# Optimization experiments

Hardware: AMD Instinct MI355X
Metric: run time of the kernel (lower is better)

The kernel has to match this reference:

```python
import jax, jax.numpy as jnp
import numpy as np

N, E, D, C, H1 = 50000, 800000, 128, 8, 2


def setup_inputs() -> dict:
    key = jax.random.key(0)
    ks = jax.random.split(key, 14)
    s = lambda k, sh: (jax.random.normal(k, sh, jnp.float32) * 0.05)
    return {
        "x": jax.random.normal(ks[0], (N, D), jnp.float32),
        "edge_index": jax.random.randint(ks[1], (2, E), 0, N, dtype=jnp.int32),
        # conv1: GATConv(D, D, heads=2, concat=True)
        "W1": s(ks[2], (D, H1 * D)),
        "att1_src": s(ks[3], (H1, D)),
        "att1_dst": s(ks[4], (H1, D)),
        "b1": s(ks[5], (H1 * D,)),
        # conv2: GATConv(2D, D, heads=1, concat=False)
        "W2": s(ks[6], (H1 * D, D)),
        "att2_src": s(ks[7], (1, D)),
        "att2_dst": s(ks[8], (1, D)),
        "b2": s(ks[9], (D,)),
        # MLP head
        "Wm1": s(ks[10], (D, D)),
        "bm1": s(ks[11], (D,)),
        "Wm2": s(ks[12], (D, C)),
        "bm2": s(ks[13], (C,)),
    }


def gat_conv(x, src, dst, W, a_src, a_dst, b, heads, out_ch, concat):
    """PyG GATConv (eval mode): self-loops added by caller, softmax over
    edges grouped by destination node, negative_slope=0.2."""
    n = x.shape[0]
    h = (x @ W).reshape(n, heads, out_ch)              # [N,H,F]
    alpha_src = jnp.einsum('nhf,hf->nh', h, a_src)     # [N,H]
    alpha_dst = jnp.einsum('nhf,hf->nh', h, a_dst)     # [N,H]
    e = jax.nn.leaky_relu(alpha_src[src] + alpha_dst[dst], 0.2)  # [E,H]
    e_max = jax.ops.segment_max(e, dst, num_segments=n)
    ex = jnp.exp(e - e_max[dst])
    denom = jax.ops.segment_sum(ex, dst, num_segments=n)
    alpha = ex / jnp.maximum(denom[dst], 1e-16)        # [E,H]
    out = jax.ops.segment_sum(h[src] * alpha[:, :, None], dst, num_segments=n)
    out = out.reshape(n, heads * out_ch) if concat else out.mean(axis=1)
    return out + b


def reference(x, edge_index, W1, att1_src, att1_dst, b1,
              W2, att2_src, att2_dst, b2, Wm1, bm1, Wm2, bm2):
    n = x.shape[0]
    loop = jnp.arange(n, dtype=edge_index.dtype)
    src = jnp.concatenate([edge_index[0], loop])  # add_self_loops=True
    dst = jnp.concatenate([edge_index[1], loop])
    h = jax.nn.elu(gat_conv(x, src, dst, W1, att1_src, att1_dst, b1, H1, D, True))
    h = jax.nn.elu(gat_conv(h, src, dst, W2, att2_src, att2_dst, b2, 1, D, False))
    h = jax.nn.relu(h @ Wm1 + bm1)
    return jax.nn.relu(h @ Wm2 + bm2)
```

## Files before the change

### kernel.cpp

```cpp
#include <hip/hip_runtime.h>
#include <hip/hip_bf16.h>


__device__ __forceinline__ float lrelu(float x){ return x > 0.f ? x : 0.2f*x; }
__device__ __forceinline__ float elu_f(float x){ return x > 0.f ? x : __expf(x) - 1.f; }
__device__ __forceinline__ unsigned short f2bf(float f){
  __hip_bfloat16 h = __float2bfloat16(f);
  return *reinterpret_cast<unsigned short*>(&h);
}
__device__ __forceinline__ float bflo(unsigned int u){ return __uint_as_float(u << 16); }
__device__ __forceinline__ float bfhi(unsigned int u){ return __uint_as_float(u & 0xffff0000u); }
__device__ __forceinline__ unsigned int packbf(float a, float b){
  return (unsigned int)f2bf(a) | ((unsigned int)f2bf(b) << 16);
}

typedef __attribute__((ext_vector_type(8))) short bf16x8;
typedef __attribute__((ext_vector_type(4))) float f32x4;

__global__ void prep_kernel(const float* __restrict__ W1, unsigned short* __restrict__ BT1a,
                            unsigned short* __restrict__ BT1b,
                            const float* __restrict__ W2, unsigned short* __restrict__ BT2,
                            const float* __restrict__ Wm1, unsigned short* __restrict__ BT3,
                            const float* __restrict__ a1s, const float* __restrict__ a1d,
                            float* __restrict__ va, int* __restrict__ bcount,
                            int* __restrict__ gcur, int NB){
  int idx = blockIdx.x*256 + threadIdx.x;
  const int S1 = 128*256, S2 = 128*256, S3 = 128*128;
  if (idx < S1){
    int k = idx >> 8, c = idx & 255;
    unsigned short v = f2bf(W1[idx]);
    if (c < 128) BT1a[c*128 + k] = v;
    else         BT1b[(c-128)*128 + k] = v;
  } else if (idx < S1 + S2){
    int j = idx - S1;
    int k = j >> 7, n = j & 127;
    BT2[n*256 + k] = f2bf(W2[j]);
  } else if (idx < S1 + S2 + S3){
    int j = idx - S1 - S2;
    int k = j >> 7, n = j & 127;
    BT3[n*128 + k] = f2bf(Wm1[j]);
  } else if (idx < S1 + S2 + S3 + 512){
    int j = idx - S1 - S2 - S3;
    int v = j >> 7, k = j & 127;
    const float* avec = (v < 2) ? a1s : a1d;
    int head = v & 1;
    const float4* wrow = (const float4*)(W1 + (size_t)k*256 + head*128);
    const float4* arow = (const float4*)(avec + head*128);
    float s = 0.f;
    #pragma unroll 8
    for (int f = 0; f < 32; ++f){
      float4 w = wrow[f], a = arow[f];
      s += w.x*a.x + w.y*a.y + w.z*a.z + w.w*a.w;
    }
    va[j] = s;
  } else if (idx < S1 + S2 + S3 + 512 + 2048){
    int z = idx - (S1 + S2 + S3 + 512);
    if (z < 1024){ if (z < NB) bcount[z] = 0; }
    else { z -= 1024; if (z < NB) gcur[z] = 0; }
  }
}

__global__ __launch_bounds__(256) void f2bf_hist_kernel(
    const float* __restrict__ x, unsigned short* __restrict__ xb, int N,
    const float* __restrict__ va, float* __restrict__ as1, float* __restrict__ ad1,
    const int* __restrict__ dst, int E, int* __restrict__ bcount, int NB, int nbConv)
{
  __shared__ int h[1024];
  if ((int)blockIdx.x < nbConv){
    int i = blockIdx.x*256 + threadIdx.x;
    int total = N*32;
    float4 v = make_float4(0.f,0.f,0.f,0.f);
    if (i < total){
      v = ((const float4*)x)[i];
      ushort4 u; u.x=f2bf(v.x); u.y=f2bf(v.y); u.z=f2bf(v.z); u.w=f2bf(v.w);
      ((ushort4*)xb)[i] = u;
    }
    int c = (i & 31) << 2;
    float4 vs0 = *(const float4*)(va + c);
    float4 vs1 = *(const float4*)(va + 128 + c);
    float4 vd0 = *(const float4*)(va + 256 + c);
    float4 vd1 = *(const float4*)(va + 384 + c);
    float s0 = v.x*vs0.x + v.y*vs0.y + v.z*vs0.z + v.w*vs0.w;
    float s1 = v.x*vs1.x + v.y*vs1.y + v.z*vs1.z + v.w*vs1.w;
    float d0 = v.x*vd0.x + v.y*vd0.y + v.z*vd0.z + v.w*vd0.w;
    float d1 = v.x*vd1.x + v.y*vd1.y + v.z*vd1.z + v.w*vd1.w;
    #pragma unroll
    for (int m = 1; m <= 16; m <<= 1){
      s0 += __shfl_xor(s0, m); s1 += __shfl_xor(s1, m);
      d0 += __shfl_xor(d0, m); d1 += __shfl_xor(d1, m);
    }
    if ((i & 31) == 0 && i < total){
      int n = i >> 5;
      *(float2*)(as1 + 2*n) = make_float2(s0, s1);
      *(float2*)(ad1 + 2*n) = make_float2(d0, d1);
    }
  } else {
    for (int i = threadIdx.x; i < NB; i += 256) h[i] = 0;
    __syncthreads();
    int b0 = blockIdx.x - nbConv;
    for (int e = b0*256 + threadIdx.x; e < E; e += 64*256)
      atomicAdd(&h[dst[e] >> 6], 1);
    __syncthreads();
    for (int i = threadIdx.x; i < NB; i += 256)
      if (h[i]) atomicAdd(&bcount[i], h[i]);
  }
}

__global__ __launch_bounds__(256) void bscatter_kernel(
    const int* __restrict__ src, const int* __restrict__ dst, int E,
    const int* __restrict__ bcount, int* __restrict__ boff,
    int* __restrict__ gcur, unsigned int* __restrict__ pairs, int NB)
{
  __shared__ int h[1024];
  __shared__ int runbase[1024];
  __shared__ int sc[1024];
  const int t = threadIdx.x;
  const int e0 = blockIdx.x * 4096;

  for (int i = t; i < 1024; i += 256) sc[i] = (i < NB) ? bcount[i] : 0;
  for (int i = t; i < NB; i += 256) h[i] = 0;
  __syncthreads();
  for (int d = 1; d < 1024; d <<= 1){
    int v0 = (t       >= d) ? sc[t       - d] : 0;
    int v1 = (t + 256 >= d) ? sc[t + 256 - d] : 0;
    int v2 = (t + 512 >= d) ? sc[t + 512 - d] : 0;
    int v3 = (t + 768 >= d) ? sc[t + 768 - d] : 0;
    __syncthreads();
    sc[t] += v0; sc[t+256] += v1; sc[t+512] += v2; sc[t+768] += v3;
    __syncthreads();
  }
  if (blockIdx.x == 0){
    for (int i = t; i <= NB; i += 256) boff[i] = i ? sc[i-1] : 0;
  }

  int myb[16]; unsigned int myw[16];
  #pragma unroll
  for (int q = 0; q < 16; ++q){
    int e = e0 + q*256 + t;
    int b = -1; unsigned int w = 0;
    if (e < E){
      int d = dst[e];
      b = d >> 6;
      w = ((unsigned int)(d & 63) << 26) | (unsigned int)src[e];
      atomicAdd(&h[b], 1);
    }
    myb[q] = b; myw[q] = w;
  }
  __syncthreads();
  for (int i = t; i < NB; i += 256)
    runbase[i] = h[i] ? atomicAdd(&gcur[i], h[i]) : 0;
  __syncthreads();
  for (int i = t; i < NB; i += 256) h[i] = 0;
  __syncthreads();
  #pragma unroll
  for (int q = 0; q < 16; ++q){
    if (myb[q] >= 0){
      int off = atomicAdd(&h[myb[q]], 1);
      int base = myb[q] ? sc[myb[q]-1] : 0;
      pairs[(size_t)base + runbase[myb[q]] + off] = myw[q];
    }
  }
}

__global__ __launch_bounds__(256) void bbuild_kernel(
    const unsigned int* __restrict__ pairs, const int* __restrict__ boff,
    int* __restrict__ rowptr, int* __restrict__ csr, int N)
{
  __shared__ int deg[64], offs[64], cur[64];
  const int b = blockIdx.x;
  const int t = threadIdx.x;
  const int n0 = b << 6;
  const int nNodes = min(64, N - n0);
  const int p0 = boff[b], p1 = boff[b+1];
  const int base = p0 + n0;
  if (t < 64) deg[t] = (t < nNodes) ? 1 : 0;
  __syncthreads();
  for (int i = p0 + t; i < p1; i += 256)
    atomicAdd(&deg[pairs[i] >> 26], 1);
  __syncthreads();
  if (t < 64){
    int x = deg[t];
    #pragma unroll
    for (int d = 1; d < 64; d <<= 1){
      int y = __shfl_up(x, d);
      if (t >= d) x += y;
    }
    offs[t] = x - deg[t];
    cur[t] = 1;
    if (t < nNodes){
      rowptr[n0 + t + 1] = base + x;
      csr[base + x - deg[t]] = n0 + t;
    }
    if (b == 0 && t == 0) rowptr[0] = 0;
  }
  __syncthreads();
  for (int i = p0 + t; i < p1; i += 256){
    unsigned int w = pairs[i];
    int dl = w >> 26;
    int s  = (int)(w & 0x03ffffffu);
    int off = atomicAdd(&cur[dl], 1);
    csr[base + offs[dl] + off] = s;
  }
}

__device__ __forceinline__ void gemm_core(
    const unsigned short* __restrict__ A, int lda,
    const unsigned short* __restrict__ BT, int M, int K, int r0,
    unsigned short* a_s, unsigned short* b_s, f32x4 (&acc)[4][4])
{
  const int tid  = threadIdx.x;
  const int lane = tid & 63, wv = tid >> 6;
  const int mh = (wv & 1)*64, nh = (wv >> 1)*64;
  const int l15 = lane & 15, quad = lane >> 4;
  const int srow = tid >> 3, skc = tid & 7;

  #pragma unroll
  for (int i = 0; i < 4; ++i)
    #pragma unroll
    for (int j = 0; j < 4; ++j)
      #pragma unroll
      for (int r = 0; r < 4; ++r) acc[i][j][r] = 0.f;

  for (int k0 = 0; k0 < K; k0 += 64){
    #pragma unroll
    for (int it = 0; it < 4; ++it){
      int row = it*32 + srow;
      int grow = r0 + row;
      uint4 v = make_uint4(0u,0u,0u,0u);
      if (grow < M) v = *(const uint4*)(A + (size_t)grow*lda + k0 + skc*8);
      *(uint4*)(&a_s[row*72 + skc*8]) = v;
    }
    #pragma unroll
    for (int it = 0; it < 4; ++it){
      int row = it*32 + srow;
      uint4 v = *(const uint4*)(BT + (size_t)row*K + k0 + skc*8);
      *(uint4*)(&b_s[row*72 + skc*8]) = v;
    }
    __syncthreads();
    #pragma unroll
    for (int ks = 0; ks < 64; ks += 32){
      bf16x8 af[4], bfr[4];
      #pragma unroll
      for (int i = 0; i < 4; ++i)
        af[i] = *(const bf16x8*)(&a_s[(mh + i*16 + l15)*72 + ks + quad*8]);
      #pragma unroll
      for (int j = 0; j < 4; ++j)
        bfr[j] = *(const bf16x8*)(&b_s[(nh + j*16 + l15)*72 + ks + quad*8]);
      #pragma unroll
      for (int i = 0; i < 4; ++i)
        #pragma unroll
        for (int j = 0; j < 4; ++j)
          acc[i][j] = __builtin_amdgcn_mfma_f32_16x16x32_bf16(bfr[j], af[i], acc[i][j], 0, 0, 0);
    }
    __syncthreads();
  }
}

__global__ __launch_bounds__(512, 2) void gemm_conv12_kernel(
    const unsigned short* __restrict__ xa,
    const unsigned short* __restrict__ BT1a, const unsigned short* __restrict__ BT1b,
    const float* __restrict__ b1, const unsigned short* __restrict__ BT2,
    unsigned short* __restrict__ h2b, int M,
    const float* __restrict__ a2s, const float* __restrict__ a2d,
    float* __restrict__ as2, float* __restrict__ ad2)
{
  __shared__ unsigned short t_s[64*264];
  __shared__ unsigned short a_s[64*72];
  __shared__ unsigned short b_s[128*72];
  __shared__ float part_s[64][4];
  __shared__ float part_d[64][4];

  const int tid = threadIdx.x;
  const int lane = tid & 63, wv = tid >> 6;
  const int l15 = lane & 15, quad = lane >> 4;
  const int r0 = blockIdx.x*64;
  const int mh = (wv & 1)*32;
  const int nhp = (wv >> 1)*32;

  const int arow = tid >> 3, askc = tid & 7;
  const int brow = tid >> 2, bc2 = (tid & 3)*2;
  #pragma unroll
  for (int h = 0; h < 2; ++h){
    const unsigned short* BT = h ? BT1b : BT1a;
    f32x4 acc[2][2];
    #pragma unroll
    for (int i = 0; i < 2; ++i)
      #pragma unroll
      for (int j = 0; j < 2; ++j)
        #pragma unroll
        for (int r = 0; r < 4; ++r) acc[i][j][r] = 0.f;

    for (int k0 = 0; k0 < 128; k0 += 64){
      {
        int grow = r0 + arow;
        uint4 v = make_uint4(0u,0u,0u,0u);
        if (grow < M) v = *(const uint4*)(xa + (size_t)grow*256 + h*128 + k0 + askc*8);
        *(uint4*)(&a_s[arow*72 + askc*8]) = v;
      }
      {
        *(uint4*)(&b_s[brow*72 + bc2*8])     = *(const uint4*)(BT + (size_t)brow*128 + k0 + bc2*8);
        *(uint4*)(&b_s[brow*72 + (bc2+1)*8]) = *(const uint4*)(BT + (size_t)brow*128 + k0 + (bc2+1)*8);
      }
      __syncthreads();
      #pragma unroll
      for (int ks = 0; ks < 64; ks += 32){
        bf16x8 af[2], bfr[2];
        #pragma unroll
        for (int i = 0; i < 2; ++i)
          af[i] = *(const bf16x8*)(&a_s[(mh + i*16 + l15)*72 + ks + quad*8]);
        #pragma unroll
        for (int j = 0; j < 2; ++j)
          bfr[j] = *(const bf16x8*)(&b_s[(nhp + j*16 + l15)*72 + ks + quad*8]);
        #pragma unroll
        for (int i = 0; i < 2; ++i)
          #pragma unroll
          for (int j = 0; j < 2; ++j)
            acc[i][j] = __builtin_amdgcn_mfma_f32_16x16x32_bf16(bfr[j], af[i], acc[i][j], 0, 0, 0);
      }
      __syncthreads();
    }
    #pragma unroll
    for (int i = 0; i < 2; ++i){
      int row = mh + i*16 + l15;
      #pragma unroll
      for (int j = 0; j < 2; ++j){
        int n = nhp + j*16 + quad*4;
        float4 bb = *(const float4*)(b1 + h*128 + n);
        ushort4 u;
        u.x = f2bf(elu_f(acc[i][j][0] + bb.x));
        u.y = f2bf(elu_f(acc[i][j][1] + bb.y));
        u.z = f2bf(elu_f(acc[i][j][2] + bb.z));
        u.w = f2bf(elu_f(acc[i][j][3] + bb.w));
        *(ushort4*)(&t_s[row*264 + h*128 + n]) = u;
      }
    }
  }
  __syncthreads();

  f32x4 acc2[2][2];
  #pragma unroll
  for (int i = 0; i < 2; ++i)
    #pragma unroll
    for (int j = 0; j < 2; ++j)
      #pragma unroll
      for (int r = 0; r < 4; ++r) acc2[i][j][r] = 0.f;

  for (int k0 = 0; k0 < 256; k0 += 64){
    {
      *(uint4*)(&b_s[brow*72 + bc2*8])     = *(const uint4*)(BT2 + (size_t)brow*256 + k0 + bc2*8);
      *(uint4*)(&b_s[brow*72 + (bc2+1)*8]) = *(const uint4*)(BT2 + (size_t)brow*256 + k0 + (bc2+1)*8);
    }
    __syncthreads();
    #pragma unroll
    for (int ks = 0; ks < 64; ks += 32){
      bf16x8 af[2], bfr[2];
      #pragma unroll
      for (int i = 0; i < 2; ++i)
        af[i] = *(const bf16x8*)(&t_s[(mh + i*16 + l15)*264 + k0 + ks + quad*8]);
      #pragma unroll
      for (int j = 0; j < 2; ++j)
        bfr[j] = *(const bf16x8*)(&b_s[(nhp + j*16 + l15)*72 + ks + quad*8]);
      #pragma unroll
      for (int i = 0; i < 2; ++i)
        #pragma unroll
        for (int j = 0; j < 2; ++j)
          acc2[i][j] = __builtin_amdgcn_mfma_f32_16x16x32_bf16(bfr[j], af[i], acc2[i][j], 0, 0, 0);
    }
    __syncthreads();
  }

  #pragma unroll
  for (int i = 0; i < 2; ++i){
    int m = r0 + mh + i*16 + l15;
    float ps = 0.f, pd = 0.f;
    #pragma unroll
    for (int j = 0; j < 2; ++j){
      int n = nhp + j*16 + quad*4;
      float4 wsv = *(const float4*)(a2s + n);
      float4 wdv = *(const float4*)(a2d + n);
      float v0 = acc2[i][j][0], v1 = acc2[i][j][1], v2 = acc2[i][j][2], v3 = acc2[i][j][3];
      ps += v0*wsv.x + v1*wsv.y + v2*wsv.z + v3*wsv.w;
      pd += v0*wdv.x + v1*wdv.y + v2*wdv.z + v3*wdv.w;
      if (m < M){
        ushort4 u;
        u.x = f2bf(v0); u.y = f2bf(v1); u.z = f2bf(v2); u.w = f2bf(v3);
        *(ushort4*)(h2b + (size_t)m*128 + n) = u;
      }
    }
    ps += __shfl_xor(ps, 16); ps += __shfl_xor(ps, 32);
    pd += __shfl_xor(pd, 16); pd += __shfl_xor(pd, 32);
    if (quad == 0){
      part_s[mh + i*16 + l15][wv >> 1] = ps;
      part_d[mh + i*16 + l15][wv >> 1] = pd;
    }
  }
  __syncthreads();
  if (tid < 64){
    int gm = r0 + tid;
    if (gm < M){
      as2[gm] = part_s[tid][0] + part_s[tid][1] + part_s[tid][2] + part_s[tid][3];
      ad2[gm] = part_d[tid][0] + part_d[tid][1] + part_d[tid][2] + part_d[tid][3];
    }
  }
}

__global__ __launch_bounds__(256) void gemm_mlp_kernel(
    const unsigned short* __restrict__ gb, const unsigned short* __restrict__ BT3,
    int M, const float* __restrict__ bm1, const float* __restrict__ Wm2,
    const float* __restrict__ bm2, float* __restrict__ out)
{
  __shared__ unsigned short a_s[128*72];
  __shared__ unsigned short b_s[128*72];
  __shared__ float wm2_s[128*8];
  __shared__ float part[128][2][8];
  const int tid = threadIdx.x;
  {
    int i4 = tid*4;
    *(float4*)(&wm2_s[i4]) = *(const float4*)(Wm2 + i4);
  }
  const int r0 = blockIdx.y*128;
  f32x4 acc[4][4];
  gemm_core(gb, 128, BT3, M, 128, r0, a_s, b_s, acc);

  const int lane = tid & 63, wv = tid >> 6;
  const int mh = (wv & 1)*64, nh = (wv >> 1)*64;
  const int l15 = lane & 15, quad = lane >> 4;
  #pragma unroll
  for (int i = 0; i < 4; ++i){
    float po[8];
    #pragma unroll
    for (int o = 0; o < 8; ++o) po[o] = 0.f;
    #pragma unroll
    for (int j = 0; j < 4; ++j){
      int n = nh + j*16 + quad*4;
      float4 bb = *(const float4*)(bm1 + n);
      #pragma unroll
      for (int r = 0; r < 4; ++r){
        float hcol = fmaxf(acc[i][j][r] + ((const float*)&bb)[r], 0.f);
        const float* wr = &wm2_s[(n + r)*8];
        #pragma unroll
        for (int o = 0; o < 8; ++o) po[o] += hcol*wr[o];
      }
    }
    #pragma unroll
    for (int o = 0; o < 8; ++o){
      po[o] += __shfl_xor(po[o], 16);
      po[o] += __shfl_xor(po[o], 32);
    }
    if (quad == 0){
      #pragma unroll
      for (int o = 0; o < 8; ++o) part[mh + i*16 + l15][wv >> 1][o] = po[o];
    }
  }
  __syncthreads();
  if (tid < 128){
    int gm = r0 + tid;
    if (gm < M){
      float4 o0, o1;
      o0.x = fmaxf(part[tid][0][0] + part[tid][1][0] + bm2[0], 0.f);
      o0.y = fmaxf(part[tid][0][1] + part[tid][1][1] + bm2[1], 0.f);
      o0.z = fmaxf(part[tid][0][2] + part[tid][1][2] + bm2[2], 0.f);
      o0.w = fmaxf(part[tid][0][3] + part[tid][1][3] + bm2[3], 0.f);
      o1.x = fmaxf(part[tid][0][4] + part[tid][1][4] + bm2[4], 0.f);
      o1.y = fmaxf(part[tid][0][5] + part[tid][1][5] + bm2[5], 0.f);
      o1.z = fmaxf(part[tid][0][6] + part[tid][1][6] + bm2[6], 0.f);
      o1.w = fmaxf(part[tid][0][7] + part[tid][1][7] + bm2[7], 0.f);
      *(float4*)(out + (size_t)gm*8)     = o0;
      *(float4*)(out + (size_t)gm*8 + 4) = o1;
    }
  }
}

#define AGG1_FMA(u, a0v, a1v) do{ \
    float f0 = bflo(u.x), f1 = bfhi(u.x), f2v = bflo(u.y), f3 = bfhi(u.y); \
    float f4 = bflo(u.z), f5 = bfhi(u.z), f6 = bflo(u.w), f7 = bfhi(u.w); \
    acc0[0] += a0v*f0; acc0[1] += a0v*f1; acc0[2] += a0v*f2v; acc0[3] += a0v*f3; \
    acc0[4] += a0v*f4; acc0[5] += a0v*f5; acc0[6] += a0v*f6;  acc0[7] += a0v*f7; \
    acc1[0] += a1v*f0; acc1[1] += a1v*f1; acc1[2] += a1v*f2v; acc1[3] += a1v*f3; \
    acc1[4] += a1v*f4; acc1[5] += a1v*f5; acc1[6] += a1v*f6;  acc1[7] += a1v*f7; \
  }while(0)

#define AGG2_FMA(u, av) do{ \
    acc[0] += av*bflo(u.x); acc[1] += av*bfhi(u.x); \
    acc[2] += av*bflo(u.y); acc[3] += av*bfhi(u.y); \
    acc[4] += av*bflo(u.z); acc[5] += av*bfhi(u.z); \
    acc[6] += av*bflo(u.w); acc[7] += av*bfhi(u.w); \
  }while(0)

__global__ __launch_bounds__(256) void agg1x_kernel(
    const unsigned short* __restrict__ xb, const float* __restrict__ as_,
    const float* __restrict__ ad_, const int* __restrict__ rowptr, const int* __restrict__ csr,
    unsigned short* __restrict__ xa, int N)
{
  const int wv = threadIdx.x >> 6, lane = threadIdx.x & 63;
  const int ql = lane & 15;
  const int n = blockIdx.x*16 + wv*4 + (lane >> 4);
  const bool valid = n < N;
  int start = 0, end = 0;
  float2 adv = make_float2(0.f, 0.f);
  if (valid){ start = rowptr[n]; end = rowptr[n+1]; adv = *(const float2*)(ad_ + 2*n); }

  int jl = start + ql;
  bool have = valid && (jl < end);
  int s_l = 0;
  float p0 = 0.f, p1 = 0.f;
  if (have){
    s_l = csr[jl];
    float2 av = *(const float2*)(as_ + 2*s_l);
    p0 = __expf(lrelu(av.x + adv.x));
    p1 = __expf(lrelu(av.y + adv.y));
  }
  float l0 = p0, l1 = p1;
  for (int j = jl + 16; j < end; j += 16){
    int s = csr[j];
    float2 av = *(const float2*)(as_ + 2*s);
    l0 += __expf(lrelu(av.x + adv.x));
    l1 += __expf(lrelu(av.y + adv.y));
  }
  #pragma unroll
  for (int msk = 1; msk <= 8; msk <<= 1){
    l0 += __shfl_xor(l0, msk);
    l1 += __shfl_xor(l1, msk);
  }
  float inv0 = 1.f / fmaxf(l0, 1e-16f);
  float inv1 = 1.f / fmaxf(l1, 1e-16f);
  float a0_l = p0 * inv0;
  float a1_l = p1 * inv1;

  float acc0[8], acc1[8];
  #pragma unroll
  for (int i = 0; i < 8; ++i){ acc0[i] = 0.f; acc1[i] = 0.f; }
  const int c = ql << 3;
  const unsigned short* hp = xb + c;

  #pragma unroll
  for (int half = 0; half < 2; ++half){
    uint4 u[8]; float b0[8], b1[8];
    #pragma unroll
    for (int t = 0; t < 8; ++t){
      int tt = half*8 + t;
      int sA = __shfl(s_l, tt, 16);
      b0[t] = __shfl(a0_l, tt, 16);
      b1[t] = __shfl(a1_l, tt, 16);
      u[t] = *(const uint4*)(hp + (sA << 7));
    }
    #pragma unroll
    for (int t = 0; t < 8; ++t) AGG1_FMA(u[t], b0[t], b1[t]);
  }
  for (int jb = start + 16; jb < end; jb += 16){
    int jl2 = jb + ql;
    int s2 = 0; float a0_2 = 0.f, a1_2 = 0.f;
    if (jl2 < end){
      s2 = csr[jl2];
      float2 av = *(const float2*)(as_ + 2*s2);
      a0_2 = __expf(lrelu(av.x + adv.x)) * inv0;
      a1_2 = __expf(lrelu(av.y + adv.y)) * inv1;
    }
    int cnt2 = min(16, end - jb);
    for (int t2 = 0; t2 < cnt2; t2 += 2){
      int   sA  = __shfl(s2, t2, 16),   sB  = __shfl(s2, t2+1, 16);
      float a0A = __shfl(a0_2, t2, 16), a0B = __shfl(a0_2, t2+1, 16);
      float a1A = __shfl(a1_2, t2, 16), a1B = __shfl(a1_2, t2+1, 16);
      uint4 uA = *(const uint4*)(hp + (sA << 7));
      uint4 uB = *(const uint4*)(hp + (sB << 7));
      AGG1_FMA(uA, a0A, a1A);
      AGG1_FMA(uB, a0B, a1B);
    }
  }

  if (valid){
    uint4 u0, u1;
    u0.x = packbf(acc0[0], acc0[1]); u0.y = packbf(acc0[2], acc0[3]);
    u0.z = packbf(acc0[4], acc0[5]); u0.w = packbf(acc0[6], acc0[7]);
    u1.x = packbf(acc1[0], acc1[1]); u1.y = packbf(acc1[2], acc1[3]);
    u1.z = packbf(acc1[4], acc1[5]); u1.w = packbf(acc1[6], acc1[7]);
    *(uint4*)(xa + (size_t)n*256 + c)       = u0;
    *(uint4*)(xa + (size_t)n*256 + 128 + c) = u1;
  }
}

__global__ __launch_bounds__(256) void agg2_kernel(
    const unsigned short* __restrict__ h2b, const float* __restrict__ as_,
    const float* __restrict__ ad_, const int* __restrict__ rowptr, const int* __restrict__ csr,
    const float* __restrict__ b2, unsigned short* __restrict__ outb, int N)
{
  const int wv = threadIdx.x >> 6, lane = threadIdx.x & 63;
  const int ql = lane & 15;
  const int n = blockIdx.x*16 + wv*4 + (lane >> 4);
  const bool valid = n < N;
  int start = 0, end = 0;
  float adn = 0.f;
  if (valid){ start = rowptr[n]; end = rowptr[n+1]; adn = ad_[n]; }

  int jl = start + ql;
  bool have = valid && (jl < end);
  int s_l = 0;
  float p_l = 0.f;
  if (have){
    s_l = csr[jl];
    p_l = __expf(lrelu(as_[s_l] + adn));
  }
  float l = p_l;
  for (int j = jl + 16; j < end; j += 16)
    l += __expf(lrelu(as_[csr[j]] + adn));
  #pragma unroll
  for (int msk = 1; msk <= 8; msk <<= 1) l += __shfl_xor(l, msk);
  float inv = 1.f / fmaxf(l, 1e-16f);
  float a_l = p_l * inv;

  float acc[8];
  #pragma unroll
  for (int i = 0; i < 8; ++i) acc[i] = 0.f;
  const int c = ql << 3;
  const unsigned short* hp = h2b + c;

  #pragma unroll
  for (int half = 0; half < 2; ++half){
    uint4 u[8]; float av[8];
    #pragma unroll
    for (int t = 0; t < 8; ++t){
      int tt = half*8 + t;
      int sA = __shfl(s_l, tt, 16);
      av[t] = __shfl(a_l, tt, 16);
      u[t] = *(const uint4*)(hp + (sA << 7));
    }
    #pragma unroll
    for (int t = 0; t < 8; ++t) AGG2_FMA(u[t], av[t]);
  }
  for (int jb = start + 16; jb < end; jb += 16){
    int jl2 = jb + ql;
    int s2 = 0; float a2 = 0.f;
    if (jl2 < end){
      s2 = csr[jl2];
      a2 = __expf(lrelu(as_[s2] + adn)) * inv;
    }
    int cnt2 = min(16, end - jb);
    for (int t2 = 0; t2 < cnt2; t2 += 2){
      int   sA = __shfl(s2, t2, 16),  sB = __shfl(s2, t2+1, 16);
      float aA = __shfl(a2, t2, 16),  aB = __shfl(a2, t2+1, 16);
      uint4 uA = *(const uint4*)(hp + (sA << 7));
      uint4 uB = *(const uint4*)(hp + (sB << 7));
      AGG2_FMA(uA, aA);
      AGG2_FMA(uB, aB);
    }
  }

  if (valid){
    float4 bb0 = *(const float4*)(b2 + c);
    float4 bb1 = *(const float4*)(b2 + c + 4);
    float o[8];
    o[0]=elu_f(acc[0]+bb0.x); o[1]=elu_f(acc[1]+bb0.y);
    o[2]=elu_f(acc[2]+bb0.z); o[3]=elu_f(acc[3]+bb0.w);
    o[4]=elu_f(acc[4]+bb1.x); o[5]=elu_f(acc[5]+bb1.y);
    o[6]=elu_f(acc[6]+bb1.z); o[7]=elu_f(acc[7]+bb1.w);
    uint4 up;
    up.x = packbf(o[0], o[1]); up.y = packbf(o[2], o[3]);
    up.z = packbf(o[4], o[5]); up.w = packbf(o[6], o[7]);
    *(uint4*)(outb + (size_t)n*128 + c) = up;
  }
}

extern "C" void kernel_launch(void* const* d_in, const int* in_sizes, int n_in,
                              void* d_out, int out_size, void* d_ws, size_t ws_size,
                              hipStream_t stream)
{
  (void)n_in; (void)out_size; (void)ws_size;
  const float* x   = (const float*)d_in[0];
  const int*   ei  = (const int*)d_in[1];
  const float* W1  = (const float*)d_in[2];
  const float* a1s = (const float*)d_in[3];
  const float* a1d = (const float*)d_in[4];
  const float* b1  = (const float*)d_in[5];
  const float* W2  = (const float*)d_in[6];
  const float* a2s = (const float*)d_in[7];
  const float* a2d = (const float*)d_in[8];
  const float* b2  = (const float*)d_in[9];
  const float* Wm1 = (const float*)d_in[10];
  const float* bm1 = (const float*)d_in[11];
  const float* Wm2 = (const float*)d_in[12];
  const float* bm2 = (const float*)d_in[13];
  float* out = (float*)d_out;

  const int N = in_sizes[0] / 128;
  const int E = in_sizes[1] / 2;
  const int NB = (N + 63) >> 6;
  const int* srcp = ei;
  const int* dstp = ei + E;

  char* ws = (char*)d_ws;
  unsigned short* xb    = (unsigned short*)ws;
  unsigned short* xa    = (unsigned short*)(ws + (size_t)N*256);
  unsigned short* h2b   = (unsigned short*)(ws + (size_t)N*768);
  char* tail = ws + (size_t)N*1024;
  unsigned short* BT1a = (unsigned short*)tail;
  unsigned short* BT1b = BT1a + 128*128;
  unsigned short* BT2  = BT1b + 128*128;
  unsigned short* BT3  = BT2 + 128*256;
  float* va   = (float*)(BT3 + 128*128);
  float* as1  = va + 512;
  float* ad1  = as1 + (size_t)2*N;
  float* as2  = ad1 + (size_t)2*N;
  float* ad2  = as2 + N;
  int* bcount = (int*)(ad2 + N);
  int* boff   = bcount + 1024;
  int* gcur   = boff + 1032;
  int* rowptr = gcur + 1024;
  int* csr    = rowptr + N + 1;
  unsigned int* pairs = (unsigned int*)(csr + E + N);

  unsigned short* gb = xb;

  const int nbConv = (N*32 + 255)/256;
  const int prepTotal = 128*256 + 128*256 + 128*128 + 512 + 2048;

  prep_kernel<<<(prepTotal + 255)/256, 256, 0, stream>>>(
      W1, BT1a, BT1b, W2, BT2, Wm1, BT3, a1s, a1d, va, bcount, gcur, NB);
  f2bf_hist_kernel<<<nbConv + 64, 256, 0, stream>>>(x, xb, N, va, as1, ad1,
                                                    dstp, E, bcount, NB, nbConv);
  bscatter_kernel<<<(E + 4095)/4096, 256, 0, stream>>>(srcp, dstp, E, bcount, boff, gcur, pairs, NB);
  bbuild_kernel<<<NB, 256, 0, stream>>>(pairs, boff, rowptr, csr, N);

  const int nb16 = (N + 15) / 16;
  const int g64  = (N + 63) / 64;
  const int gy   = (N + 127) / 128;

  agg1x_kernel<<<nb16, 256, 0, stream>>>(xb, as1, ad1, rowptr, csr, xa, N);
  gemm_conv12_kernel<<<g64, 512, 0, stream>>>(xa, BT1a, BT1b, b1, BT2,
                                              h2b, N, a2s, a2d, as2, ad2);
  agg2_kernel<<<nb16, 256, 0, stream>>>(h2b, as2, ad2, rowptr, csr, b2, gb, N);
  gemm_mlp_kernel<<<dim3(1, gy), 256, 0, stream>>>(gb, BT3, N, bm1, Wm2, bm2, out);
}
```

Measured before the change: 250.9 us.

## Fuse second-layer aggregation with MLP head into a single kernel

Merges the conv2 aggregation kernel and the MLP GEMM kernel. Each 16-node block now writes its ELU'd bf16 features to shared memory and immediately runs a small MFMA GEMM against Wm1, followed by the Wm2 projection. This removes the global write and re-read of the intermediate feature matrix and one kernel launch. In exchange, every block re-reads Wm1 (BT3) from global/L2, the 16-row MFMA tiles are less efficient, and extra shared memory per block may lower occupancy.

```diff
diff --git a/kernel.cpp b/kernel.cpp
--- a/kernel.cpp
+++ b/kernel.cpp
@@ -203,59 +203,6 @@
   }
 }
 
-__device__ __forceinline__ void gemm_core(
-    const unsigned short* __restrict__ A, int lda,
-    const unsigned short* __restrict__ BT, int M, int K, int r0,
-    unsigned short* a_s, unsigned short* b_s, f32x4 (&acc)[4][4])
-{
-  const int tid  = threadIdx.x;
-  const int lane = tid & 63, wv = tid >> 6;
-  const int mh = (wv & 1)*64, nh = (wv >> 1)*64;
-  const int l15 = lane & 15, quad = lane >> 4;
-  const int srow = tid >> 3, skc = tid & 7;
-
-  #pragma unroll
-  for (int i = 0; i < 4; ++i)
-    #pragma unroll
-    for (int j = 0; j < 4; ++j)
-      #pragma unroll
-      for (int r = 0; r < 4; ++r) acc[i][j][r] = 0.f;
-
-  for (int k0 = 0; k0 < K; k0 += 64){
-    #pragma unroll
-    for (int it = 0; it < 4; ++it){
-      int row = it*32 + srow;
-      int grow = r0 + row;
-      uint4 v = make_uint4(0u,0u,0u,0u);
-      if (grow < M) v = *(const uint4*)(A + (size_t)grow*lda + k0 + skc*8);
-      *(uint4*)(&a_s[row*72 + skc*8]) = v;
-    }
-    #pragma unroll
-    for (int it = 0; it < 4; ++it){
-      int row = it*32 + srow;
-      uint4 v = *(const uint4*)(BT + (size_t)row*K + k0 + skc*8);
-      *(uint4*)(&b_s[row*72 + skc*8]) = v;
-    }
-    __syncthreads();
-    #pragma unroll
-    for (int ks = 0; ks < 64; ks += 32){
-      bf16x8 af[4], bfr[4];
-      #pragma unroll
-      for (int i = 0; i < 4; ++i)
-        af[i] = *(const bf16x8*)(&a_s[(mh + i*16 + l15)*72 + ks + quad*8]);
-      #pragma unroll
-      for (int j = 0; j < 4; ++j)
-        bfr[j] = *(const bf16x8*)(&b_s[(nh + j*16 + l15)*72 + ks + quad*8]);
-      #pragma unroll
-      for (int i = 0; i < 4; ++i)
-        #pragma unroll
-        for (int j = 0; j < 4; ++j)
-          acc[i][j] = __builtin_amdgcn_mfma_f32_16x16x32_bf16(bfr[j], af[i], acc[i][j], 0, 0, 0);
-    }
-    __syncthreads();
-  }
-}
-
 __global__ __launch_bounds__(512, 2) void gemm_conv12_kernel(
     const unsigned short* __restrict__ xa,
     const unsigned short* __restrict__ BT1a, const unsigned short* __restrict__ BT1b,
@@ -404,73 +351,6 @@
   }
 }
 
-__global__ __launch_bounds__(256) void gemm_mlp_kernel(
-    const unsigned short* __restrict__ gb, const unsigned short* __restrict__ BT3,
-    int M, const float* __restrict__ bm1, const float* __restrict__ Wm2,
-    const float* __restrict__ bm2, float* __restrict__ out)
-{
-  __shared__ unsigned short a_s[128*72];
-  __shared__ unsigned short b_s[128*72];
-  __shared__ float wm2_s[128*8];
-  __shared__ float part[128][2][8];
-  const int tid = threadIdx.x;
-  {
-    int i4 = tid*4;
-    *(float4*)(&wm2_s[i4]) = *(const float4*)(Wm2 + i4);
-  }
-  const int r0 = blockIdx.y*128;
-  f32x4 acc[4][4];
-  gemm_core(gb, 128, BT3, M, 128, r0, a_s, b_s, acc);
-
-  const int lane = tid & 63, wv = tid >> 6;
-  const int mh = (wv & 1)*64, nh = (wv >> 1)*64;
-  const int l15 = lane & 15, quad = lane >> 4;
-  #pragma unroll
-  for (int i = 0; i < 4; ++i){
-    float po[8];
-    #pragma unroll
-    for (int o = 0; o < 8; ++o) po[o] = 0.f;
-    #pragma unroll
-    for (int j = 0; j < 4; ++j){
-      int n = nh + j*16 + quad*4;
-      float4 bb = *(const float4*)(bm1 + n);
-      #pragma unroll
-      for (int r = 0; r < 4; ++r){
-        float hcol = fmaxf(acc[i][j][r] + ((const float*)&bb)[r], 0.f);
-        const float* wr = &wm2_s[(n + r)*8];
-        #pragma unroll
-        for (int o = 0; o < 8; ++o) po[o] += hcol*wr[o];
-      }
-    }
-    #pragma unroll
-    for (int o = 0; o < 8; ++o){
-      po[o] += __shfl_xor(po[o], 16);
-      po[o] += __shfl_xor(po[o], 32);
-    }
-    if (quad == 0){
-      #pragma unroll
-      for (int o = 0; o < 8; ++o) part[mh + i*16 + l15][wv >> 1][o] = po[o];
-    }
-  }
-  __syncthreads();
-  if (tid < 128){
-    int gm = r0 + tid;
-    if (gm < M){
-      float4 o0, o1;
-      o0.x = fmaxf(part[tid][0][0] + part[tid][1][0] + bm2[0], 0.f);
-      o0.y = fmaxf(part[tid][0][1] + part[tid][1][1] + bm2[1], 0.f);
-      o0.z = fmaxf(part[tid][0][2] + part[tid][1][2] + bm2[2], 0.f);
-      o0.w = fmaxf(part[tid][0][3] + part[tid][1][3] + bm2[3], 0.f);
-      o1.x = fmaxf(part[tid][0][4] + part[tid][1][4] + bm2[4], 0.f);
-      o1.y = fmaxf(part[tid][0][5] + part[tid][1][5] + bm2[5], 0.f);
-      o1.z = fmaxf(part[tid][0][6] + part[tid][1][6] + bm2[6], 0.f);
-      o1.w = fmaxf(part[tid][0][7] + part[tid][1][7] + bm2[7], 0.f);
-      *(float4*)(out + (size_t)gm*8)     = o0;
-      *(float4*)(out + (size_t)gm*8 + 4) = o1;
-    }
-  }
-}
-
 #define AGG1_FMA(u, a0v, a1v) do{ \
     float f0 = bflo(u.x), f1 = bfhi(u.x), f2v = bflo(u.y), f3 = bfhi(u.y); \
     float f4 = bflo(u.z), f5 = bfhi(u.z), f6 = bflo(u.w), f7 = bfhi(u.w); \
@@ -579,14 +459,25 @@
   }
 }
 
-__global__ __launch_bounds__(256) void agg2_kernel(
+__global__ __launch_bounds__(256, 4) void agg2mlp_kernel(
     const unsigned short* __restrict__ h2b, const float* __restrict__ as_,
     const float* __restrict__ ad_, const int* __restrict__ rowptr, const int* __restrict__ csr,
-    const float* __restrict__ b2, unsigned short* __restrict__ outb, int N)
+    const float* __restrict__ b2, const unsigned short* __restrict__ BT3,
+    const float* __restrict__ bm1, const float* __restrict__ Wm2,
+    const float* __restrict__ bm2, float* __restrict__ out, int N)
 {
-  const int wv = threadIdx.x >> 6, lane = threadIdx.x & 63;
+  __shared__ unsigned short gb_s[16*136];
+  __shared__ float wm2_s[128*8];
+  __shared__ float part[16][4][8];
+  const int tid = threadIdx.x;
+  {
+    int i4 = tid*4;
+    *(float4*)(&wm2_s[i4]) = *(const float4*)(Wm2 + i4);
+  }
+  const int wv = tid >> 6, lane = tid & 63;
   const int ql = lane & 15;
-  const int n = blockIdx.x*16 + wv*4 + (lane >> 4);
+  const int g = wv*4 + (lane >> 4);
+  const int n = blockIdx.x*16 + g;
   const bool valid = n < N;
   int start = 0, end = 0;
   float adn = 0.f;
@@ -645,7 +536,7 @@
     }
   }
 
-  if (valid){
+  {
     float4 bb0 = *(const float4*)(b2 + c);
     float4 bb1 = *(const float4*)(b2 + c + 4);
     float o[8];
@@ -656,7 +547,68 @@
     uint4 up;
     up.x = packbf(o[0], o[1]); up.y = packbf(o[2], o[3]);
     up.z = packbf(o[4], o[5]); up.w = packbf(o[6], o[7]);
-    *(uint4*)(outb + (size_t)n*128 + c) = up;
+    *(uint4*)(&gb_s[g*136 + c]) = up;
+  }
+  __syncthreads();
+
+  const int l15 = lane & 15, quad = lane >> 4;
+  const int nh = wv*32;
+  f32x4 macc[2];
+  #pragma unroll
+  for (int j = 0; j < 2; ++j)
+    #pragma unroll
+    for (int r = 0; r < 4; ++r) macc[j][r] = 0.f;
+
+  #pragma unroll
+  for (int ks = 0; ks < 128; ks += 32){
+    bf16x8 af = *(const bf16x8*)(&gb_s[l15*136 + ks + quad*8]);
+    #pragma unroll
+    for (int j = 0; j < 2; ++j){
+      bf16x8 bfr = *(const bf16x8*)(BT3 + (size_t)(nh + j*16 + l15)*128 + ks + quad*8);
+      macc[j] = __builtin_amdgcn_mfma_f32_16x16x32_bf16(bfr, af, macc[j], 0, 0, 0);
+    }
+  }
+
+  float po[8];
+  #pragma unroll
+  for (int o = 0; o < 8; ++o) po[o] = 0.f;
+  #pragma unroll
+  for (int j = 0; j < 2; ++j){
+    int nn = nh + j*16 + quad*4;
+    float4 bb = *(const float4*)(bm1 + nn);
+    #pragma unroll
+    for (int r = 0; r < 4; ++r){
+      float hcol = fmaxf(macc[j][r] + ((const float*)&bb)[r], 0.f);
+      const float* wr = &wm2_s[(nn + r)*8];
+      #pragma unroll
+      for (int o = 0; o < 8; ++o) po[o] += hcol*wr[o];
+    }
+  }
+  #pragma unroll
+  for (int o = 0; o < 8; ++o){
+    po[o] += __shfl_xor(po[o], 16);
+    po[o] += __shfl_xor(po[o], 32);
+  }
+  if (quad == 0){
+    #pragma unroll
+    for (int o = 0; o < 8; ++o) part[l15][wv][o] = po[o];
+  }
+  __syncthreads();
+  if (tid < 16){
+    int gm = blockIdx.x*16 + tid;
+    if (gm < N){
+      float4 o0, o1;
+      o0.x = fmaxf(part[tid][0][0]+part[tid][1][0]+part[tid][2][0]+part[tid][3][0] + bm2[0], 0.f);
+      o0.y = fmaxf(part[tid][0][1]+part[tid][1][1]+part[tid][2][1]+part[tid][3][1] + bm2[1], 0.f);
+      o0.z = fmaxf(part[tid][0][2]+part[tid][1][2]+part[tid][2][2]+part[tid][3][2] + bm2[2], 0.f);
+      o0.w = fmaxf(part[tid][0][3]+part[tid][1][3]+part[tid][2][3]+part[tid][3][3] + bm2[3], 0.f);
+      o1.x = fmaxf(part[tid][0][4]+part[tid][1][4]+part[tid][2][4]+part[tid][3][4] + bm2[4], 0.f);
+      o1.y = fmaxf(part[tid][0][5]+part[tid][1][5]+part[tid][2][5]+part[tid][3][5] + bm2[5], 0.f);
+      o1.z = fmaxf(part[tid][0][6]+part[tid][1][6]+part[tid][2][6]+part[tid][3][6] + bm2[6], 0.f);
+      o1.w = fmaxf(part[tid][0][7]+part[tid][1][7]+part[tid][2][7]+part[tid][3][7] + bm2[7], 0.f);
+      *(float4*)(out + (size_t)gm*8)     = o0;
+      *(float4*)(out + (size_t)gm*8 + 4) = o1;
+    }
   }
 }
 
@@ -708,8 +660,6 @@
   int* csr    = rowptr + N + 1;
   unsigned int* pairs = (unsigned int*)(csr + E + N);
 
-  unsigned short* gb = xb;
-
   const int nbConv = (N*32 + 255)/256;
   const int prepTotal = 128*256 + 128*256 + 128*128 + 512 + 2048;
 
@@ -722,11 +672,10 @@
 
   const int nb16 = (N + 15) / 16;
   const int g64  = (N + 63) / 64;
-  const int gy   = (N + 127) / 128;
 
   agg1x_kernel<<<nb16, 256, 0, stream>>>(xb, as1, ad1, rowptr, csr, xa, N);
   gemm_conv12_kernel<<<g64, 512, 0, stream>>>(xa, BT1a, BT1b, b1, BT2,
                                               h2b, N, a2s, a2d, as2, ad2);
-  agg2_kernel<<<nb16, 256, 0, stream>>>(h2b, as2, ad2, rowptr, csr, b2, gb, N);
-  gemm_mlp_kernel<<<dim3(1, gy), 256, 0, stream>>>(gb, BT3, N, bm1, Wm2, bm2, out);
-}
+  agg2mlp_kernel<<<nb16, 256, 0, stream>>>(h2b, as2, ad2, rowptr, csr,
+                                           b2, BT3, bm1, Wm2, bm2, out, N);
+}
```

New measurement: 252.2 us. Within noise of the previous version (+0.5%).
